# Kernel optimization log

Measured on AMD Instinct MI355X. Metric: run time of the kernel, lower is better.

Reference implementation:

```python
import jax, jax.numpy as jnp
import numpy as np

NUM_PAIRS, PAIR_DIM, MACRO_DIM, NUM_SLOTS, BATCH = 28, 128, 256, 64, 4096
D_ALL = NUM_PAIRS * PAIR_DIM  # 3584
EPS = 1e-5


def _layernorm(x, g, b):
    mu = jnp.mean(x, axis=-1, keepdims=True)
    var = jnp.mean(jnp.square(x - mu), axis=-1, keepdims=True)
    return (x - mu) * jax.lax.rsqrt(var + EPS) * g + b


def _memory_read(q, keys, values):
    # attention-style associative read: softmax(q K^T / sqrt(dk)) V
    dk = keys.shape[-1]
    scores = jnp.einsum('bd,sd->bs', q, keys) / jnp.sqrt(jnp.asarray(dk, q.dtype))
    attn = jax.nn.softmax(scores, axis=-1)
    return jnp.einsum('bs,sv->bv', attn, values)


def setup_inputs() -> dict:
    key = jax.random.key(0)
    ks = jax.random.split(key, 12)
    s = lambda k, shape, scale=0.02: jax.random.normal(k, shape, dtype=jnp.float32) * scale
    return {
        'pair_states': jax.random.normal(ks[0], (BATCH, NUM_PAIRS, PAIR_DIM), dtype=jnp.float32),
        'macro_state': jax.random.normal(ks[1], (BATCH, MACRO_DIM), dtype=jnp.float32),
        'mem_pair_keys': s(ks[2], (NUM_SLOTS, PAIR_DIM)),
        'mem_pair_vals': s(ks[3], (NUM_SLOTS, D_ALL)),
        'mem_macro_keys': s(ks[4], (NUM_SLOTS, MACRO_DIM)),
        'mem_macro_vals': s(ks[5], (NUM_SLOTS, D_ALL)),
        'fusion_w1': s(ks[6], (2 * D_ALL, D_ALL)),
        'fusion_b1': jnp.zeros((D_ALL,), jnp.float32),
        'fusion_ln_g': jnp.ones((D_ALL,), jnp.float32),
        'fusion_ln_b': jnp.zeros((D_ALL,), jnp.float32),
        'fusion_w2': s(ks[7], (D_ALL, D_ALL)),
        'fusion_b2': jnp.zeros((D_ALL,), jnp.float32),
        'pair_w': s(ks[8], (NUM_PAIRS, 2 * PAIR_DIM, PAIR_DIM)),
        'pair_b': jnp.zeros((NUM_PAIRS, PAIR_DIM), jnp.float32),
        'pair_ln_g': jnp.ones((NUM_PAIRS, PAIR_DIM), jnp.float32),
        'pair_ln_b': jnp.zeros((NUM_PAIRS, PAIR_DIM), jnp.float32),
    }


def reference(pair_states, macro_state, mem_pair_keys, mem_pair_vals,
              mem_macro_keys, mem_macro_vals, fusion_w1, fusion_b1,
              fusion_ln_g, fusion_ln_b, fusion_w2, fusion_b2,
              pair_w, pair_b, pair_ln_g, pair_ln_b):
    B = pair_states.shape[0]
    # associative memory reads
    pair_query = jnp.mean(pair_states, axis=1)                       # (B, pair_dim)
    pair_corr = _memory_read(pair_query, mem_pair_keys, mem_pair_vals)   # (B, D_ALL)
    macro_corr = _memory_read(macro_state, mem_macro_keys, mem_macro_vals)  # (B, D_ALL)
    # fusion MLP: Linear -> LayerNorm -> GELU -> Linear
    h = jnp.concatenate([pair_corr, macro_corr], axis=-1) @ fusion_w1 + fusion_b1
    h = jax.nn.gelu(_layernorm(h, fusion_ln_g, fusion_ln_b), approximate=False)
    fused = (h @ fusion_w2 + fusion_b2).reshape(B, NUM_PAIRS, PAIR_DIM)
    # per-pair Linear + LayerNorm, batched over the pair axis
    x = jnp.concatenate([pair_states, fused], axis=-1)               # (B, P, 2*pair_dim)
    out = jnp.einsum('bpd,pde->bpe', x, pair_w) + pair_b
    return _layernorm(out, pair_ln_g, pair_ln_b)
```

## Files before the change

### kernel.cpp

```cpp
#include <hip/hip_runtime.h>
#include <hip/hip_bf16.h>
#include <math.h>


#define B_SZ  4096
#define NPAIR 28
#define PDIM  128
#define MDIM  256
#define NSLOT 64
#define DALL  3584
#define DCAT  7168
#define KS2   16
#define KCH2  448

typedef __hip_bfloat16 bf16;
typedef __attribute__((ext_vector_type(8))) short bf16x8;
typedef __attribute__((ext_vector_type(4))) float f32x4;

#define BARRIER() asm volatile("s_barrier" ::: "memory")
#define VMCNT4()  asm volatile("s_waitcnt vmcnt(4)" ::: "memory")
#define VMCNT0()  asm volatile("s_waitcnt vmcnt(0)" ::: "memory")

__device__ __forceinline__ void async_copy16(void* lds, const void* g) {
  __builtin_amdgcn_global_load_lds((__attribute__((address_space(1))) void*)g,
                                   (__attribute__((address_space(3))) void*)lds,
                                   16, 0, 0);
}

template <int OUT_BF16, int ADD_BIAS>
__global__ __launch_bounds__(512, 2)
void gemm8(const bf16* __restrict__ A, int lda, const bf16* __restrict__ Bt,
           int ldb, void* __restrict__ Cout, int ldc,
           const float* __restrict__ bias, int K, int nbx) {
  __shared__ __align__(16) char smem[131072];
  const int tid = threadIdx.x;
  const int wid = tid >> 6, lane = tid & 63;
  const int lr = lane & 15, lk = lane >> 4;
  const int wm = wid >> 2, wn = wid & 3;
  const int nwg = gridDim.x, cpx = nwg >> 3;
  const int swz = ((int)blockIdx.x & 7) * cpx + ((int)blockIdx.x >> 3);
  const int bx = swz % nbx, by = swz / nbx;
  const int col0 = bx * 256, row0 = by * 256;

  char* sA = smem;
  char* sB = smem + 65536;

  const int srow = tid >> 3;
  const int sg = (tid & 7) ^ (srow & 7);
  const bf16* aStage = A + (long)(row0 + srow) * lda + sg * 8;
  const bf16* bStage = Bt + (long)(col0 + srow) * ldb + sg * 8;
  const int wOff = wid << 10;

  const int NT = K >> 6;

  const int sx = lr & 7;
  const int arow = wm * 128 + lr;
  const int brow = wn * 64 + lr;

  f32x4 acc[8][4];
  const f32x4 zero = {0.f, 0.f, 0.f, 0.f};
#pragma unroll
  for (int m = 0; m < 8; ++m)
#pragma unroll
    for (int n = 0; n < 4; ++n) acc[m][n] = zero;

#pragma unroll
  for (int h = 0; h < 2; ++h) {
    const bf16* g = bStage + (long)h * 128 * ldb;
    char* d = sB + h * 16384 + wOff;
    async_copy16(d, g);
    async_copy16(d + 8192, g + 64 * ldb);
  }
#pragma unroll
  for (int h = 0; h < 2; ++h) {
    const bf16* g = aStage + (long)h * 128 * lda;
    char* d = sA + h * 16384 + wOff;
    async_copy16(d, g);
    async_copy16(d + 8192, g + 64 * lda);
  }
#pragma unroll
  for (int h = 0; h < 2; ++h) {
    const bf16* g = bStage + (long)h * 128 * ldb + 64;
    char* d = sB + 32768 + h * 16384 + wOff;
    async_copy16(d, g);
    async_copy16(d + 8192, g + 64 * ldb);
  }
  VMCNT4();
  BARRIER();

  bf16x8 af[4][2], bl[2][2], bh[2][2];

  for (int t = 0; t < NT; ++t) {
    const int buf = t & 1;
    char* cA = sA + buf * 32768;
    char* cB = sB + buf * 32768;
    char* nA = sA + (buf ^ 1) * 32768;

    if (t + 1 < NT) {
      const bf16* g = aStage + (long)(t + 1) * 64;
      async_copy16(nA + wOff, g);
      async_copy16(nA + 8192 + wOff, g + 64 * lda);
    }
#pragma unroll
    for (int m = 0; m < 4; ++m)
#pragma unroll
      for (int kk = 0; kk < 2; ++kk)
        af[m][kk] = *(const bf16x8*)(cA + (arow + m * 16) * 128 +
                                     ((((kk << 2) | lk) ^ sx) << 4));
#pragma unroll
    for (int n = 0; n < 2; ++n)
#pragma unroll
      for (int kk = 0; kk < 2; ++kk)
        bl[n][kk] = *(const bf16x8*)(cB + (brow + n * 16) * 128 +
                                     ((((kk << 2) | lk) ^ sx) << 4));
    __builtin_amdgcn_s_setprio(1);
#pragma unroll
    for (int m = 0; m < 4; ++m)
#pragma unroll
      for (int n = 0; n < 2; ++n)
#pragma unroll
        for (int kk = 0; kk < 2; ++kk)
          acc[m][n] = __builtin_amdgcn_mfma_f32_16x16x32_bf16(
              af[m][kk], bl[n][kk], acc[m][n], 0, 0, 0);
    __builtin_amdgcn_s_setprio(0);
    BARRIER();

    if (t + 1 < NT) {
      const bf16* g = aStage + (long)128 * lda + (long)(t + 1) * 64;
      async_copy16(nA + 16384 + wOff, g);
      async_copy16(nA + 16384 + 8192 + wOff, g + 64 * lda);
    }
#pragma unroll
    for (int n = 0; n < 2; ++n)
#pragma unroll
      for (int kk = 0; kk < 2; ++kk)
        bh[n][kk] = *(const bf16x8*)(cB + (brow + (n + 2) * 16) * 128 +
                                     ((((kk << 2) | lk) ^ sx) << 4));
    __builtin_amdgcn_s_setprio(1);
#pragma unroll
    for (int m = 0; m < 4; ++m)
#pragma unroll
      for (int n = 0; n < 2; ++n)
#pragma unroll
        for (int kk = 0; kk < 2; ++kk)
          acc[m][n + 2] = __builtin_amdgcn_mfma_f32_16x16x32_bf16(
              af[m][kk], bh[n][kk], acc[m][n + 2], 0, 0, 0);
    __builtin_amdgcn_s_setprio(0);
    BARRIER();

    if (t + 2 < NT) {
      const bf16* g = bStage + (long)(t + 2) * 64;
      async_copy16(cB + wOff, g);
      async_copy16(cB + 8192 + wOff, g + 64 * ldb);
    }
#pragma unroll
    for (int m = 0; m < 4; ++m)
#pragma unroll
      for (int kk = 0; kk < 2; ++kk)
        af[m][kk] = *(const bf16x8*)(cA + (arow + (m + 4) * 16) * 128 +
                                     ((((kk << 2) | lk) ^ sx) << 4));
    __builtin_amdgcn_s_setprio(1);
#pragma unroll
    for (int m = 0; m < 4; ++m)
#pragma unroll
      for (int n = 0; n < 2; ++n)
#pragma unroll
        for (int kk = 0; kk < 2; ++kk)
          acc[m + 4][n] = __builtin_amdgcn_mfma_f32_16x16x32_bf16(
              af[m][kk], bl[n][kk], acc[m + 4][n], 0, 0, 0);
    __builtin_amdgcn_s_setprio(0);
    BARRIER();

    const int more = (t + 2 < NT);
    if (more) {
      const bf16* g = bStage + (long)128 * ldb + (long)(t + 2) * 64;
      async_copy16(cB + 16384 + wOff, g);
      async_copy16(cB + 16384 + 8192 + wOff, g + 64 * ldb);
    }
    __builtin_amdgcn_s_setprio(1);
#pragma unroll
    for (int m = 0; m < 4; ++m)
#pragma unroll
      for (int n = 0; n < 2; ++n)
#pragma unroll
        for (int kk = 0; kk < 2; ++kk)
          acc[m + 4][n + 2] = __builtin_amdgcn_mfma_f32_16x16x32_bf16(
              af[m][kk], bh[n][kk], acc[m + 4][n + 2], 0, 0, 0);
    __builtin_amdgcn_s_setprio(0);
    if (more) { VMCNT4(); } else { VMCNT0(); }
    BARRIER();
  }

#pragma unroll
  for (int m = 0; m < 8; ++m) {
#pragma unroll
    for (int n = 0; n < 4; ++n) {
      const int gc = col0 + wn * 64 + n * 16 + lr;
      const float bia = ADD_BIAS ? bias[gc] : 0.f;
#pragma unroll
      for (int j = 0; j < 4; ++j) {
        const int gr = row0 + wm * 128 + m * 16 + lk * 4 + j;
        const float v = acc[m][n][j] + bia;
        const long off = (long)gr * ldc + gc;
        if (OUT_BF16)
          ((bf16*)Cout)[off] = __float2bfloat16(v);
        else
          ((float*)Cout)[off] = v;
      }
    }
  }
}

__global__ __launch_bounds__(256)
void tconv_kernel(const float* __restrict__ in, bf16* __restrict__ out,
                  int R, int C, int inBatch, int outBatch) {
  __shared__ float tile[32][33];
  const int tid = threadIdx.x;
  const int tx = tid & 31, ty = tid >> 5;
  const long ib = (long)blockIdx.z * inBatch;
  const long ob = (long)blockIdx.z * outBatch;
  const int c0 = blockIdx.x * 32, r0 = blockIdx.y * 32;
#pragma unroll
  for (int i = 0; i < 4; ++i)
    tile[ty + i * 8][tx] = in[ib + (long)(r0 + ty + i * 8) * C + c0 + tx];
  __syncthreads();
#pragma unroll
  for (int i = 0; i < 4; ++i)
    out[ob + (long)(c0 + ty + i * 8) * R + r0 + tx] =
        __float2bfloat16(tile[tx][ty + i * 8]);
}

__global__ __launch_bounds__(256)
void conv_kernel(const float* __restrict__ in, bf16* __restrict__ out, int n) {
  const int i = (blockIdx.x * 256 + threadIdx.x) * 8;
  if (i + 7 < n) {
    float4 a = *(const float4*)(in + i);
    float4 b = *(const float4*)(in + i + 4);
    bf16 o[8];
    o[0] = __float2bfloat16(a.x); o[1] = __float2bfloat16(a.y);
    o[2] = __float2bfloat16(a.z); o[3] = __float2bfloat16(a.w);
    o[4] = __float2bfloat16(b.x); o[5] = __float2bfloat16(b.y);
    o[6] = __float2bfloat16(b.z); o[7] = __float2bfloat16(b.w);
    *(bf16x8*)(out + i) = *(bf16x8*)o;
  }
}

__global__ __launch_bounds__(256)
void prep_kernel(const bf16* __restrict__ psb, const float* __restrict__ mac,
                 const float* __restrict__ pkeys, const float* __restrict__ mkeys,
                 bf16* __restrict__ att) {
  const int b = blockIdx.x, tid = threadIdx.x;
  __shared__ float q[PDIM];
  __shared__ float mrow[MDIM];
  if (tid < MDIM) mrow[tid] = mac[(long)b * MDIM + tid];
  if (tid < PDIM) {
    const bf16* prow = psb + (long)b * DALL + tid;
    float s = 0.f;
#pragma unroll
    for (int p = 0; p < NPAIR; ++p) s += __bfloat162float(prow[p * PDIM]);
    q[tid] = s * (1.f / NPAIR);
  }
  __syncthreads();
  const int wid = tid >> 6, lane = tid & 63;
  if (wid == 0) {
    float sc = 0.f;
    const float* kr = pkeys + lane * PDIM;
    for (int d = 0; d < PDIM; ++d) sc += q[d] * kr[d];
    sc *= 0.08838834764831845f;
    float mx = sc;
#pragma unroll
    for (int m = 32; m; m >>= 1) mx = fmaxf(mx, __shfl_xor(mx, m));
    float e = expf(sc - mx);
    float ssum = e;
#pragma unroll
    for (int m = 32; m; m >>= 1) ssum += __shfl_xor(ssum, m);
    att[(long)b * 128 + lane] = __float2bfloat16(e / ssum);
  } else if (wid == 1) {
    float sc = 0.f;
    const float* kr = mkeys + lane * MDIM;
    for (int d = 0; d < MDIM; ++d) sc += mrow[d] * kr[d];
    sc *= 0.0625f;
    float mx = sc;
#pragma unroll
    for (int m = 32; m; m >>= 1) mx = fmaxf(mx, __shfl_xor(mx, m));
    float e = expf(sc - mx);
    float ssum = e;
#pragma unroll
    for (int m = 32; m; m >>= 1) ssum += __shfl_xor(ssum, m);
    att[(long)b * 128 + 64 + lane] = __float2bfloat16(e / ssum);
  }
}

__global__ __launch_bounds__(256)
void precompute_direct(const float* __restrict__ w1, const bf16* __restrict__ pvb,
                       const bf16* __restrict__ mvb, float* __restrict__ part) {
  __shared__ __align__(16) bf16 sAt[256 * 40];
  __shared__ __align__(16) bf16 sBt[64 * 32];
  const int tid = threadIdx.x, wid = tid >> 6, lane = tid & 63;
  const int lr = lane & 15, lk = lane >> 4;
  const int n0 = blockIdx.x * 256;
  const int ksb = blockIdx.y;
  const int kbase = ksb * KCH2;
  const bf16* vb = (ksb < 8) ? pvb : mvb;
  const int kcol0 = (ksb < 8) ? kbase : kbase - DALL;

  const int bs = tid >> 2;
  const int bgs = (tid & 3) ^ (bs & 3);

  f32x4 acc[4][4];
  const f32x4 zero = {0.f, 0.f, 0.f, 0.f};
#pragma unroll
  for (int m = 0; m < 4; ++m)
#pragma unroll
    for (int n = 0; n < 4; ++n) acc[m][n] = zero;

  for (int kt = 0; kt < KCH2; kt += 32) {
    __syncthreads();
    {
      const float* src = w1 + (long)(kbase + kt) * DALL + n0 + tid;
      bf16* dst = sAt + tid * 40;
#pragma unroll
      for (int r = 0; r < 32; ++r)
        dst[r] = __float2bfloat16(src[(long)r * DALL]);
    }
    async_copy16((char*)sBt + tid * 16,
                 vb + (long)bs * DALL + kcol0 + kt + bgs * 8);
    __syncthreads();
    bf16x8 af[4], bfr[4];
#pragma unroll
    for (int m = 0; m < 4; ++m)
      af[m] = *(const bf16x8*)((const char*)sAt +
                               ((wid * 64 + m * 16 + lr) * 40 + lk * 8) * 2);
#pragma unroll
    for (int n = 0; n < 4; ++n) {
      const int s = n * 16 + lr;
      bfr[n] = *(const bf16x8*)((const char*)sBt + s * 64 + ((lk ^ (s & 3)) << 4));
    }
#pragma unroll
    for (int m = 0; m < 4; ++m)
#pragma unroll
      for (int n = 0; n < 4; ++n)
        acc[m][n] =
            __builtin_amdgcn_mfma_f32_16x16x32_bf16(af[m], bfr[n], acc[m][n], 0, 0, 0);
  }
#pragma unroll
  for (int m = 0; m < 4; ++m)
#pragma unroll
    for (int n = 0; n < 4; ++n)
#pragma unroll
      for (int j = 0; j < 4; ++j) {
        const int gn = n0 + wid * 64 + m * 16 + lk * 4 + j;
        const int s = n * 16 + lr;
        part[((long)ksb * DALL + gn) * 64 + s] = acc[m][n][j];
      }
}

__global__ __launch_bounds__(256)
void reduce_cvt(const float* __restrict__ part, bf16* __restrict__ cvt) {
  const long i4 = ((long)blockIdx.x * 256 + threadIdx.x) * 4;
  const int n = (int)(i4 >> 7), sc = (int)(i4 & 127);
  const int half = sc >> 6, s0 = sc & 63;
  f32x4 s = {0.f, 0.f, 0.f, 0.f};
#pragma unroll
  for (int j = 0; j < 8; ++j)
    s += *(const f32x4*)(part + ((long)(half * 8 + j) * DALL + n) * 64 + s0);
#pragma unroll
  for (int k = 0; k < 4; ++k) cvt[i4 + k] = __float2bfloat16(s[k]);
}

template <int OUT_BF16, int ADD_BIAS>
__global__ __launch_bounds__(256)
void gemm_bt(const bf16* __restrict__ A, int lda, const bf16* __restrict__ Bt,
             void* __restrict__ Cout, int ldc, int col_off,
             const float* __restrict__ bias, int K) {
  __shared__ __align__(16) bf16 sA[128 * 32];
  __shared__ __align__(16) bf16 sB[128 * 32];
  const int tid = threadIdx.x;
  const int wid = tid >> 6, lane = tid & 63;
  const int lr = lane & 15, lk = lane >> 4;
  const int col0 = blockIdx.x * 128, row0 = blockIdx.y * 128;
  const int wrow = (wid >> 1) * 64, wcol = (wid & 1) * 64;
  const int ea = tid * 8;
  const int ra = ea >> 5, ca = ea & 31;

  f32x4 acc[4][4];
  const f32x4 zero = {0.f, 0.f, 0.f, 0.f};
#pragma unroll
  for (int m = 0; m < 4; ++m)
#pragma unroll
    for (int n = 0; n < 4; ++n) acc[m][n] = zero;

  const long aBase = (long)row0 * lda;
  const long bBase = (long)col0 * K;
  char* sAb = (char*)sA;
  char* sBb = (char*)sB;
  const int wOff = wid * 1024;

  for (int kt = 0; kt < K; kt += 32) {
    __syncthreads();
#pragma unroll
    for (int i = 0; i < 2; ++i) {
      async_copy16(sAb + i * 4096 + wOff,
                   A + aBase + (long)(ra + i * 64) * lda + kt + ca);
      async_copy16(sBb + i * 4096 + wOff,
                   Bt + bBase + (long)(ra + i * 64) * K + kt + ca);
    }
    __syncthreads();
    bf16x8 af[4], bfr[4];
    const bf16x8* pA = (const bf16x8*)sA;
    const bf16x8* pB = (const bf16x8*)sB;
#pragma unroll
    for (int m = 0; m < 4; ++m) af[m] = pA[(wrow + m * 16 + lr) * 4 + lk];
#pragma unroll
    for (int n = 0; n < 4; ++n) bfr[n] = pB[(wcol + n * 16 + lr) * 4 + lk];
#pragma unroll
    for (int m = 0; m < 4; ++m)
#pragma unroll
      for (int n = 0; n < 4; ++n)
        acc[m][n] =
            __builtin_amdgcn_mfma_f32_16x16x32_bf16(af[m], bfr[n], acc[m][n], 0, 0, 0);
  }
#pragma unroll
  for (int m = 0; m < 4; ++m) {
#pragma unroll
    for (int n = 0; n < 4; ++n) {
      const int gcl = col0 + wcol + n * 16 + lr;
      const float bia = ADD_BIAS ? bias[gcl] : 0.f;
#pragma unroll
      for (int j = 0; j < 4; ++j) {
        const int gr = row0 + wrow + m * 16 + lk * 4 + j;
        const float v = acc[m][n][j] + bia;
        const long off = (long)gr * ldc + col_off + gcl;
        if (OUT_BF16)
          ((bf16*)Cout)[off] = __float2bfloat16(v);
        else
          ((float*)Cout)[off] = v;
      }
    }
  }
}

__global__ __launch_bounds__(256)
void ln_gelu_kernel(const bf16* __restrict__ h, const float* __restrict__ g,
                    const float* __restrict__ bb, bf16* __restrict__ h2) {
  const int row = blockIdx.x, tid = threadIdx.x;
  const bf16* x = h + (long)row * DALL;
  float v[14];
  float s1 = 0.f, s2 = 0.f;
#pragma unroll
  for (int i = 0; i < 14; ++i) {
    v[i] = __bfloat162float(x[i * 256 + tid]);
    s1 += v[i];
    s2 += v[i] * v[i];
  }
#pragma unroll
  for (int m = 32; m; m >>= 1) {
    s1 += __shfl_xor(s1, m);
    s2 += __shfl_xor(s2, m);
  }
  __shared__ float r1[4], r2[4];
  const int wid = tid >> 6, lane = tid & 63;
  if (lane == 0) {
    r1[wid] = s1;
    r2[wid] = s2;
  }
  __syncthreads();
  s1 = r1[0] + r1[1] + r1[2] + r1[3];
  s2 = r2[0] + r2[1] + r2[2] + r2[3];
  const float mean = s1 * (1.f / DALL);
  const float var = s2 * (1.f / DALL) - mean * mean;
  const float rstd = rsqrtf(var + 1e-5f);
#pragma unroll
  for (int i = 0; i < 14; ++i) {
    const int c = i * 256 + tid;
    const float y = (v[i] - mean) * rstd * g[c] + bb[c];
    const float ge = 0.5f * y * (1.f + erff(y * 0.7071067811865475f));
    h2[(long)row * DALL + c] = __float2bfloat16(ge);
  }
}

__global__ __launch_bounds__(256)
void pair_final(const bf16* __restrict__ psb, const bf16* __restrict__ fusedb,
                const bf16* __restrict__ pwT, const float* __restrict__ pb,
                const float* __restrict__ lng, const float* __restrict__ lnb,
                float* __restrict__ out) {
  __shared__ __align__(16) bf16 sA[128 * 32];
  __shared__ __align__(16) bf16 sB[128 * 32];
  const int tid = threadIdx.x, wid = tid >> 6, lane = tid & 63;
  const int lr = lane & 15, lk = lane >> 4;
  const int p = blockIdx.y, row0 = blockIdx.x * 128;
  const int ea = tid * 8, ra = ea >> 5, ca = ea & 31;

  f32x4 acc[2][8];
  const f32x4 zero = {0.f, 0.f, 0.f, 0.f};
#pragma unroll
  for (int m = 0; m < 2; ++m)
#pragma unroll
    for (int n = 0; n < 8; ++n) acc[m][n] = zero;

  const bf16* pwp = pwT + (long)p * (PDIM * MDIM);
  char* sAb = (char*)sA;
  char* sBb = (char*)sB;
  const int wOff = wid * 1024;

  for (int kt = 0; kt < MDIM; kt += 32) {
    __syncthreads();
    const bf16* Asrc = (kt < PDIM) ? psb : fusedb;
    const int kc = kt & (PDIM - 1);
#pragma unroll
    for (int i = 0; i < 2; ++i) {
      async_copy16(sAb + i * 4096 + wOff,
                   Asrc + (long)(row0 + ra + i * 64) * DALL + p * PDIM + kc + ca);
      async_copy16(sBb + i * 4096 + wOff, pwp + (ra + i * 64) * MDIM + kt + ca);
    }
    __syncthreads();
    bf16x8 af[2], bfr[8];
    const bf16x8* pA = (const bf16x8*)sA;
    const bf16x8* pB = (const bf16x8*)sB;
#pragma unroll
    for (int m = 0; m < 2; ++m) af[m] = pA[(wid * 32 + m * 16 + lr) * 4 + lk];
#pragma unroll
    for (int n = 0; n < 8; ++n) bfr[n] = pB[(n * 16 + lr) * 4 + lk];
#pragma unroll
    for (int m = 0; m < 2; ++m)
#pragma unroll
      for (int n = 0; n < 8; ++n)
        acc[m][n] =
            __builtin_amdgcn_mfma_f32_16x16x32_bf16(af[m], bfr[n], acc[m][n], 0, 0, 0);
  }
  float g_[8], b_[8], pb_[8];
#pragma unroll
  for (int n = 0; n < 8; ++n) {
    const int c = n * 16 + lr;
    g_[n] = lng[p * PDIM + c];
    b_[n] = lnb[p * PDIM + c];
    pb_[n] = pb[p * PDIM + c];
  }
#pragma unroll
  for (int m = 0; m < 2; ++m) {
#pragma unroll
    for (int j = 0; j < 4; ++j) {
      float vv[8];
      float s1 = 0.f, s2 = 0.f;
#pragma unroll
      for (int n = 0; n < 8; ++n) {
        vv[n] = acc[m][n][j] + pb_[n];
        s1 += vv[n];
        s2 += vv[n] * vv[n];
      }
#pragma unroll
      for (int msk = 1; msk <= 8; msk <<= 1) {
        s1 += __shfl_xor(s1, msk);
        s2 += __shfl_xor(s2, msk);
      }
      const float mean = s1 * (1.f / 128.f);
      const float var = s2 * (1.f / 128.f) - mean * mean;
      const float rstd = rsqrtf(var + 1e-5f);
      const int gr = row0 + wid * 32 + m * 16 + lk * 4 + j;
      float* orow = out + ((long)gr * NPAIR + p) * PDIM;
#pragma unroll
      for (int n = 0; n < 8; ++n)
        orow[n * 16 + lr] = (vv[n] - mean) * rstd * g_[n] + b_[n];
    }
  }
}

extern "C" void kernel_launch(void* const* d_in, const int* in_sizes, int n_in,
                              void* d_out, int out_size, void* d_ws, size_t ws_size,
                              hipStream_t stream) {
  (void)in_sizes; (void)n_in; (void)out_size; (void)ws_size;
  const float* ps   = (const float*)d_in[0];
  const float* mac  = (const float*)d_in[1];
  const float* pkey = (const float*)d_in[2];
  const float* pval = (const float*)d_in[3];
  const float* mkey = (const float*)d_in[4];
  const float* mval = (const float*)d_in[5];
  const float* w1   = (const float*)d_in[6];
  const float* b1   = (const float*)d_in[7];
  const float* lng1 = (const float*)d_in[8];
  const float* lnb1 = (const float*)d_in[9];
  const float* w2   = (const float*)d_in[10];
  const float* b2   = (const float*)d_in[11];
  const float* pw   = (const float*)d_in[12];
  const float* pb   = (const float*)d_in[13];
  const float* plng = (const float*)d_in[14];
  const float* plnb = (const float*)d_in[15];
  float* out = (float*)d_out;

  char* w = (char*)d_ws;
  size_t off = 0;
  auto carve = [&](size_t bytes) {
    char* pp = w + off;
    off += (bytes + 255) & ~(size_t)255;
    return pp;
  };
  bf16* psb   = (bf16*)carve((size_t)B_SZ * DALL * 2);
  bf16* w2t   = (bf16*)carve((size_t)DALL * DALL * 2);
  bf16* pvb   = (bf16*)carve((size_t)NSLOT * DALL * 2);
  bf16* mvb   = (bf16*)carve((size_t)NSLOT * DALL * 2);
  bf16* pwTb  = (bf16*)carve((size_t)NPAIR * PDIM * MDIM * 2);
  bf16* att   = (bf16*)carve((size_t)B_SZ * 128 * 2);
  bf16* cvt   = (bf16*)carve((size_t)DALL * 128 * 2);
  float* part = (float*)carve((size_t)KS2 * DALL * 64 * 4);
  bf16* hpreb = (bf16*)carve((size_t)B_SZ * DALL * 2);
  bf16* h2    = (bf16*)carve((size_t)B_SZ * DALL * 2);
  bf16* fusedb = hpreb;

  conv_kernel<<<dim3(B_SZ * DALL / 2048), 256, 0, stream>>>(ps, psb, B_SZ * DALL);
  conv_kernel<<<dim3(NSLOT * DALL / 2048), 256, 0, stream>>>(pval, pvb, NSLOT * DALL);
  conv_kernel<<<dim3(NSLOT * DALL / 2048), 256, 0, stream>>>(mval, mvb, NSLOT * DALL);
  tconv_kernel<<<dim3(DALL / 32, DALL / 32, 1), 256, 0, stream>>>(w2, w2t, DALL, DALL, 0, 0);
  tconv_kernel<<<dim3(PDIM / 32, MDIM / 32, NPAIR), 256, 0, stream>>>(
      pw, pwTb, MDIM, PDIM, MDIM * PDIM, MDIM * PDIM);
  prep_kernel<<<dim3(B_SZ), 256, 0, stream>>>(psb, mac, pkey, mkey, att);
  precompute_direct<<<dim3(DALL / 256, KS2), 256, 0, stream>>>(w1, pvb, mvb, part);
  reduce_cvt<<<dim3(DALL * 128 / 1024), 256, 0, stream>>>(part, cvt);
  gemm_bt<1, 1><<<dim3(DALL / 128, B_SZ / 128), 256, 0, stream>>>(
      att, 128, cvt, hpreb, DALL, 0, b1, 128);
  ln_gelu_kernel<<<dim3(B_SZ), 256, 0, stream>>>(hpreb, lng1, lnb1, h2);
  gemm8<1, 1><<<dim3((DALL / 256) * (B_SZ / 256)), 512, 0, stream>>>(
      h2, DALL, w2t, DALL, fusedb, DALL, b2, DALL, DALL / 256);
  pair_final<<<dim3(B_SZ / 128, NPAIR), 256, 0, stream>>>(
      psb, fusedb, pwTb, pb, plng, plnb, out);
}
```

Baseline: 293.6 us.

## Retile second fusion GEMM to 256x224 tiles and fuse pair-state conversion into prep

Replaces the 256x256-tile GEMM for the second fusion linear with a 256x224 tile, giving 256 workgroups instead of 224 so the grid matches the CU count. Warps are rearranged to 4x2 with 4x7 MFMA fragments per warp, and the per-k-step barriers drop from four to two. The B staging still loads 256 rows per tile, so the transposed weight buffer gains 32 rows of padding to absorb the over-read. Separately, the fp32-to-bf16 conversion of pair_states moves into prep_kernel, removing one full pass over that tensor. The two memory-value conversions are also merged into one launch.

Result: faster. 283.9 us (-3.3%).

```diff
diff --git a/kernel.cpp b/kernel.cpp
--- a/kernel.cpp
+++ b/kernel.cpp
@@ -18,6 +18,7 @@
 typedef __attribute__((ext_vector_type(4))) float f32x4;
 
 #define BARRIER() asm volatile("s_barrier" ::: "memory")
+#define LGKM0()   asm volatile("s_waitcnt lgkmcnt(0)" ::: "memory")
 #define VMCNT4()  asm volatile("s_waitcnt vmcnt(4)" ::: "memory")
 #define VMCNT0()  asm volatile("s_waitcnt vmcnt(0)" ::: "memory")
 
@@ -27,185 +28,122 @@
                                    16, 0, 0);
 }
 
-template <int OUT_BF16, int ADD_BIAS>
 __global__ __launch_bounds__(512, 2)
-void gemm8(const bf16* __restrict__ A, int lda, const bf16* __restrict__ Bt,
-           int ldb, void* __restrict__ Cout, int ldc,
-           const float* __restrict__ bias, int K, int nbx) {
+void gemm224(const bf16* __restrict__ A, const bf16* __restrict__ Bt,
+             bf16* __restrict__ Cout, const float* __restrict__ bias) {
   __shared__ __align__(16) char smem[131072];
   const int tid = threadIdx.x;
   const int wid = tid >> 6, lane = tid & 63;
   const int lr = lane & 15, lk = lane >> 4;
-  const int wm = wid >> 2, wn = wid & 3;
-  const int nwg = gridDim.x, cpx = nwg >> 3;
-  const int swz = ((int)blockIdx.x & 7) * cpx + ((int)blockIdx.x >> 3);
-  const int bx = swz % nbx, by = swz / nbx;
-  const int col0 = bx * 256, row0 = by * 256;
+  const int wm = wid >> 1, wn = wid & 1;
+  const int swz = ((int)blockIdx.x & 7) * 32 + ((int)blockIdx.x >> 3);
+  const int bx = swz & 15, by = swz >> 4;
+  const int col0 = bx * 224, row0 = by * 256;
 
   char* sA = smem;
   char* sB = smem + 65536;
 
   const int srow = tid >> 3;
   const int sg = (tid & 7) ^ (srow & 7);
-  const bf16* aStage = A + (long)(row0 + srow) * lda + sg * 8;
-  const bf16* bStage = Bt + (long)(col0 + srow) * ldb + sg * 8;
+  const bf16* aStage = A + (long)(row0 + srow) * DALL + sg * 8;
+  const bf16* bStage = Bt + (long)(col0 + srow) * DALL + sg * 8;
   const int wOff = wid << 10;
 
-  const int NT = K >> 6;
+  const int NT = DALL >> 6;
 
   const int sx = lr & 7;
-  const int arow = wm * 128 + lr;
-  const int brow = wn * 64 + lr;
-
-  f32x4 acc[8][4];
+  const int arowb = wm * 64 + lr;
+  const int browb = wn * 112 + lr;
+
+  f32x4 acc[4][7];
   const f32x4 zero = {0.f, 0.f, 0.f, 0.f};
 #pragma unroll
-  for (int m = 0; m < 8; ++m)
-#pragma unroll
-    for (int n = 0; n < 4; ++n) acc[m][n] = zero;
-
-#pragma unroll
-  for (int h = 0; h < 2; ++h) {
-    const bf16* g = bStage + (long)h * 128 * ldb;
-    char* d = sB + h * 16384 + wOff;
-    async_copy16(d, g);
-    async_copy16(d + 8192, g + 64 * ldb);
-  }
-#pragma unroll
-  for (int h = 0; h < 2; ++h) {
-    const bf16* g = aStage + (long)h * 128 * lda;
-    char* d = sA + h * 16384 + wOff;
-    async_copy16(d, g);
-    async_copy16(d + 8192, g + 64 * lda);
-  }
-#pragma unroll
-  for (int h = 0; h < 2; ++h) {
-    const bf16* g = bStage + (long)h * 128 * ldb + 64;
-    char* d = sB + 32768 + h * 16384 + wOff;
-    async_copy16(d, g);
-    async_copy16(d + 8192, g + 64 * ldb);
-  }
+  for (int m = 0; m < 4; ++m)
+#pragma unroll
+    for (int n = 0; n < 7; ++n) acc[m][n] = zero;
+
+#pragma unroll
+  for (int i = 0; i < 4; ++i)
+    async_copy16(sB + i * 8192 + wOff, bStage + (long)i * 64 * DALL);
+#pragma unroll
+  for (int i = 0; i < 4; ++i)
+    async_copy16(sA + i * 8192 + wOff, aStage + (long)i * 64 * DALL);
+#pragma unroll
+  for (int i = 0; i < 4; ++i)
+    async_copy16(sB + 32768 + i * 8192 + wOff, bStage + (long)i * 64 * DALL + 64);
   VMCNT4();
   BARRIER();
 
-  bf16x8 af[4][2], bl[2][2], bh[2][2];
+  bf16x8 af[4][2], bf[7][2];
 
   for (int t = 0; t < NT; ++t) {
-    const int buf = t & 1;
-    char* cA = sA + buf * 32768;
-    char* cB = sB + buf * 32768;
-    char* nA = sA + (buf ^ 1) * 32768;
+    const int cur = t & 1;
+    char* cA = sA + cur * 32768;
+    char* cB = sB + cur * 32768;
+    char* nA = sA + (cur ^ 1) * 32768;
 
     if (t + 1 < NT) {
       const bf16* g = aStage + (long)(t + 1) * 64;
-      async_copy16(nA + wOff, g);
-      async_copy16(nA + 8192 + wOff, g + 64 * lda);
+#pragma unroll
+      for (int i = 0; i < 4; ++i)
+        async_copy16(nA + i * 8192 + wOff, g + (long)i * 64 * DALL);
     }
 #pragma unroll
     for (int m = 0; m < 4; ++m)
 #pragma unroll
       for (int kk = 0; kk < 2; ++kk)
-        af[m][kk] = *(const bf16x8*)(cA + (arow + m * 16) * 128 +
+        af[m][kk] = *(const bf16x8*)(cA + (arowb + m * 16) * 128 +
                                      ((((kk << 2) | lk) ^ sx) << 4));
 #pragma unroll
-    for (int n = 0; n < 2; ++n)
+    for (int n = 0; n < 7; ++n)
 #pragma unroll
       for (int kk = 0; kk < 2; ++kk)
-        bl[n][kk] = *(const bf16x8*)(cB + (brow + n * 16) * 128 +
+        bf[n][kk] = *(const bf16x8*)(cB + (browb + n * 16) * 128 +
                                      ((((kk << 2) | lk) ^ sx) << 4));
     __builtin_amdgcn_s_setprio(1);
 #pragma unroll
     for (int m = 0; m < 4; ++m)
 #pragma unroll
-      for (int n = 0; n < 2; ++n)
+      for (int n = 0; n < 4; ++n)
 #pragma unroll
         for (int kk = 0; kk < 2; ++kk)
           acc[m][n] = __builtin_amdgcn_mfma_f32_16x16x32_bf16(
-              af[m][kk], bl[n][kk], acc[m][n], 0, 0, 0);
+              af[m][kk], bf[n][kk], acc[m][n], 0, 0, 0);
     __builtin_amdgcn_s_setprio(0);
-    BARRIER();
-
-    if (t + 1 < NT) {
-      const bf16* g = aStage + (long)128 * lda + (long)(t + 1) * 64;
-      async_copy16(nA + 16384 + wOff, g);
-      async_copy16(nA + 16384 + 8192 + wOff, g + 64 * lda);
-    }
-#pragma unroll
-    for (int n = 0; n < 2; ++n)
-#pragma unroll
-      for (int kk = 0; kk < 2; ++kk)
-        bh[n][kk] = *(const bf16x8*)(cB + (brow + (n + 2) * 16) * 128 +
-                                     ((((kk << 2) | lk) ^ sx) << 4));
-    __builtin_amdgcn_s_setprio(1);
-#pragma unroll
-    for (int m = 0; m < 4; ++m)
-#pragma unroll
-      for (int n = 0; n < 2; ++n)
-#pragma unroll
-        for (int kk = 0; kk < 2; ++kk)
-          acc[m][n + 2] = __builtin_amdgcn_mfma_f32_16x16x32_bf16(
-              af[m][kk], bh[n][kk], acc[m][n + 2], 0, 0, 0);
-    __builtin_amdgcn_s_setprio(0);
-    BARRIER();
-
-    if (t + 2 < NT) {
-      const bf16* g = bStage + (long)(t + 2) * 64;
-      async_copy16(cB + wOff, g);
-      async_copy16(cB + 8192 + wOff, g + 64 * ldb);
-    }
-#pragma unroll
-    for (int m = 0; m < 4; ++m)
-#pragma unroll
-      for (int kk = 0; kk < 2; ++kk)
-        af[m][kk] = *(const bf16x8*)(cA + (arow + (m + 4) * 16) * 128 +
-                                     ((((kk << 2) | lk) ^ sx) << 4));
-    __builtin_amdgcn_s_setprio(1);
-#pragma unroll
-    for (int m = 0; m < 4; ++m)
-#pragma unroll
-      for (int n = 0; n < 2; ++n)
-#pragma unroll
-        for (int kk = 0; kk < 2; ++kk)
-          acc[m + 4][n] = __builtin_amdgcn_mfma_f32_16x16x32_bf16(
-              af[m][kk], bl[n][kk], acc[m + 4][n], 0, 0, 0);
-    __builtin_amdgcn_s_setprio(0);
+    LGKM0();
     BARRIER();
 
     const int more = (t + 2 < NT);
     if (more) {
-      const bf16* g = bStage + (long)128 * ldb + (long)(t + 2) * 64;
-      async_copy16(cB + 16384 + wOff, g);
-      async_copy16(cB + 16384 + 8192 + wOff, g + 64 * ldb);
+      const bf16* g = bStage + (long)(t + 2) * 64;
+#pragma unroll
+      for (int i = 0; i < 4; ++i)
+        async_copy16(cB + i * 8192 + wOff, g + (long)i * 64 * DALL);
     }
     __builtin_amdgcn_s_setprio(1);
 #pragma unroll
     for (int m = 0; m < 4; ++m)
 #pragma unroll
-      for (int n = 0; n < 2; ++n)
+      for (int n = 4; n < 7; ++n)
 #pragma unroll
         for (int kk = 0; kk < 2; ++kk)
-          acc[m + 4][n + 2] = __builtin_amdgcn_mfma_f32_16x16x32_bf16(
-              af[m][kk], bh[n][kk], acc[m + 4][n + 2], 0, 0, 0);
+          acc[m][n] = __builtin_amdgcn_mfma_f32_16x16x32_bf16(
+              af[m][kk], bf[n][kk], acc[m][n], 0, 0, 0);
     __builtin_amdgcn_s_setprio(0);
     if (more) { VMCNT4(); } else { VMCNT0(); }
     BARRIER();
   }
 
 #pragma unroll
-  for (int m = 0; m < 8; ++m) {
-#pragma unroll
-    for (int n = 0; n < 4; ++n) {
-      const int gc = col0 + wn * 64 + n * 16 + lr;
-      const float bia = ADD_BIAS ? bias[gc] : 0.f;
+  for (int m = 0; m < 4; ++m) {
+#pragma unroll
+    for (int n = 0; n < 7; ++n) {
+      const int gc = col0 + wn * 112 + n * 16 + lr;
+      const float bia = bias[gc];
 #pragma unroll
       for (int j = 0; j < 4; ++j) {
-        const int gr = row0 + wm * 128 + m * 16 + lk * 4 + j;
-        const float v = acc[m][n][j] + bia;
-        const long off = (long)gr * ldc + gc;
-        if (OUT_BF16)
-          ((bf16*)Cout)[off] = __float2bfloat16(v);
-        else
-          ((float*)Cout)[off] = v;
+        const int gr = row0 + wm * 64 + m * 16 + lk * 4 + j;
+        Cout[(long)gr * DALL + gc] = __float2bfloat16(acc[m][n][j] + bia);
       }
     }
   }
@@ -231,35 +169,38 @@
 }
 
 __global__ __launch_bounds__(256)
-void conv_kernel(const float* __restrict__ in, bf16* __restrict__ out, int n) {
+void conv2_kernel(const float* __restrict__ pv, const float* __restrict__ mv,
+                  bf16* __restrict__ pvb, bf16* __restrict__ mvb) {
+  const float* in = blockIdx.y ? mv : pv;
+  bf16* out = blockIdx.y ? mvb : pvb;
   const int i = (blockIdx.x * 256 + threadIdx.x) * 8;
-  if (i + 7 < n) {
-    float4 a = *(const float4*)(in + i);
-    float4 b = *(const float4*)(in + i + 4);
-    bf16 o[8];
-    o[0] = __float2bfloat16(a.x); o[1] = __float2bfloat16(a.y);
-    o[2] = __float2bfloat16(a.z); o[3] = __float2bfloat16(a.w);
-    o[4] = __float2bfloat16(b.x); o[5] = __float2bfloat16(b.y);
-    o[6] = __float2bfloat16(b.z); o[7] = __float2bfloat16(b.w);
-    *(bf16x8*)(out + i) = *(bf16x8*)o;
-  }
-}
-
-__global__ __launch_bounds__(256)
-void prep_kernel(const bf16* __restrict__ psb, const float* __restrict__ mac,
+  float4 a = *(const float4*)(in + i);
+  float4 b = *(const float4*)(in + i + 4);
+  bf16 o[8];
+  o[0] = __float2bfloat16(a.x); o[1] = __float2bfloat16(a.y);
+  o[2] = __float2bfloat16(a.z); o[3] = __float2bfloat16(a.w);
+  o[4] = __float2bfloat16(b.x); o[5] = __float2bfloat16(b.y);
+  o[6] = __float2bfloat16(b.z); o[7] = __float2bfloat16(b.w);
+  *(bf16x8*)(out + i) = *(bf16x8*)o;
+}
+
+__global__ __launch_bounds__(256)
+void prep_kernel(const float* __restrict__ ps, const float* __restrict__ mac,
                  const float* __restrict__ pkeys, const float* __restrict__ mkeys,
-                 bf16* __restrict__ att) {
+                 bf16* __restrict__ psb, bf16* __restrict__ att) {
   const int b = blockIdx.x, tid = threadIdx.x;
   __shared__ float q[PDIM];
   __shared__ float mrow[MDIM];
+  const float* prow = ps + (long)b * DALL;
   if (tid < MDIM) mrow[tid] = mac[(long)b * MDIM + tid];
   if (tid < PDIM) {
-    const bf16* prow = psb + (long)b * DALL + tid;
     float s = 0.f;
 #pragma unroll
-    for (int p = 0; p < NPAIR; ++p) s += __bfloat162float(prow[p * PDIM]);
+    for (int p = 0; p < NPAIR; ++p) s += prow[p * PDIM + tid];
     q[tid] = s * (1.f / NPAIR);
   }
+  for (int i = tid; i < DALL; i += 256)
+    psb[(long)b * DALL + i] = __float2bfloat16(prow[i]);
   __syncthreads();
   const int wid = tid >> 6, lane = tid & 63;
   if (wid == 0) {
@@ -595,7 +536,7 @@
     return pp;
   };
   bf16* psb   = (bf16*)carve((size_t)B_SZ * DALL * 2);
-  bf16* w2t   = (bf16*)carve((size_t)DALL * DALL * 2);
+  bf16* w2t   = (bf16*)carve((size_t)(DALL + 32) * DALL * 2);
   bf16* pvb   = (bf16*)carve((size_t)NSLOT * DALL * 2);
   bf16* mvb   = (bf16*)carve((size_t)NSLOT * DALL * 2);
   bf16* pwTb  = (bf16*)carve((size_t)NPAIR * PDIM * MDIM * 2);
@@ -606,20 +547,17 @@
   bf16* h2    = (bf16*)carve((size_t)B_SZ * DALL * 2);
   bf16* fusedb = hpreb;
 
-  conv_kernel<<<dim3(B_SZ * DALL / 2048), 256, 0, stream>>>(ps, psb, B_SZ * DALL);
-  conv_kernel<<<dim3(NSLOT * DALL / 2048), 256, 0, stream>>>(pval, pvb, NSLOT * DALL);
-  conv_kernel<<<dim3(NSLOT * DALL / 2048), 256, 0, stream>>>(mval, mvb, NSLOT * DALL);
+  conv2_kernel<<<dim3(NSLOT * DALL / 2048, 2), 256, 0, stream>>>(pval, mval, pvb, mvb);
   tconv_kernel<<<dim3(DALL / 32, DALL / 32, 1), 256, 0, stream>>>(w2, w2t, DALL, DALL, 0, 0);
   tconv_kernel<<<dim3(PDIM / 32, MDIM / 32, NPAIR), 256, 0, stream>>>(
       pw, pwTb, MDIM, PDIM, MDIM * PDIM, MDIM * PDIM);
-  prep_kernel<<<dim3(B_SZ), 256, 0, stream>>>(psb, mac, pkey, mkey, att);
+  prep_kernel<<<dim3(B_SZ), 256, 0, stream>>>(ps, mac, pkey, mkey, psb, att);
   precompute_direct<<<dim3(DALL / 256, KS2), 256, 0, stream>>>(w1, pvb, mvb, part);
   reduce_cvt<<<dim3(DALL * 128 / 1024), 256, 0, stream>>>(part, cvt);
   gemm_bt<1, 1><<<dim3(DALL / 128, B_SZ / 128), 256, 0, stream>>>(
       att, 128, cvt, hpreb, DALL, 0, b1, 128);
   ln_gelu_kernel<<<dim3(B_SZ), 256, 0, stream>>>(hpreb, lng1, lnb1, h2);
-  gemm8<1, 1><<<dim3((DALL / 256) * (B_SZ / 256)), 512, 0, stream>>>(
-      h2, DALL, w2t, DALL, fusedb, DALL, b2, DALL, DALL / 256);
+  gemm224<<<dim3(256), 512, 0, stream>>>(h2, w2t, fusedb, b2);
   pair_final<<<dim3(B_SZ / 128, NPAIR), 256, 0, stream>>>(
       psb, fusedb, pwTb, pb, plng, plnb, out);
 }
```
